# Performance work log

Measured on AMD Instinct MI355X. Metric: run time of the kernel, lower is better.

The kernel has to match this reference:

```python
import jax, jax.numpy as jnp
import numpy as np

N = 100000
IN_C, HID_C, OUT_C = 128, 128, 64
E = 1600000


def setup_inputs() -> dict:
    key = jax.random.key(0)
    ks = jax.random.split(key, 8)
    x = jax.random.normal(ks[0], (N, IN_C), dtype=jnp.float32)
    edge_index = jax.random.randint(ks[1], (2, E), 0, N, dtype=jnp.int64)
    def glorot(k, fan_in, fan_out):
        lim = np.sqrt(6.0 / (fan_in + fan_out)).astype(np.float32)
        return jax.random.uniform(k, (fan_in, fan_out), jnp.float32, -lim, lim)
    return {
        "x": x,
        "edge_index": edge_index,
        "W1l": glorot(ks[2], IN_C, HID_C),   # lin_l: aggregated neighbors
        "W1r": glorot(ks[3], IN_C, HID_C),   # lin_r: root/self
        "b1": jnp.zeros((HID_C,), jnp.float32),
        "W2l": glorot(ks[4], HID_C, OUT_C),
        "W2r": glorot(ks[5], HID_C, OUT_C),
        "b2": jnp.zeros((OUT_C,), jnp.float32),
    }


def _sage_conv(x, src, dst, Wl, Wr, b):
    # mean aggregation over incoming edges: gather source feats, segment-sum at dst
    msg_sum = jax.ops.segment_sum(x[src], dst, num_segments=N)          # [N, C_in]
    deg = jax.ops.segment_sum(jnp.ones((src.shape[0],), x.dtype), dst,
                              num_segments=N)                           # [N]
    mean = msg_sum / jnp.clip(deg, 1.0, None)[:, None]
    return mean @ Wl + x @ Wr + b


def reference(x, edge_index, W1l, W1r, b1, W2l, W2r, b2):
    src, dst = edge_index[0], edge_index[1]
    h = jax.nn.relu(_sage_conv(x, src, dst, W1l, W1r, b1))
    out = _sage_conv(h, src, dst, W2l, W2r, b2)
    return out
```

## Files before the change

### kernel.cpp

```cpp
#include <hip/hip_runtime.h>
#include <type_traits>


constexpr int K = 128;
constexpr int EB = 4096;

typedef __bf16 bf16x2 __attribute__((ext_vector_type(2)));
typedef __bf16 bf16x4 __attribute__((ext_vector_type(4)));
typedef __bf16 bf16x8 __attribute__((ext_vector_type(8)));
typedef float f32x4 __attribute__((ext_vector_type(4)));
typedef float f32x2 __attribute__((ext_vector_type(2)));


__device__ __forceinline__ unsigned char to_fp8(float v) {
#if __has_builtin(__builtin_amdgcn_cvt_pk_fp8_f32)
  int p = __builtin_amdgcn_cvt_pk_fp8_f32(v, v, 0, false);
  return (unsigned char)(p & 0xff);
#else
  unsigned u = __builtin_bit_cast(unsigned, v);
  unsigned s = (u >> 24) & 0x80u;
  float a = fabsf(v);
  if (a > 448.f) a = 448.f;
  unsigned bits;
  if (a < 0.015625f) {
    bits = (unsigned)(a * 512.f + 0.5f);
  } else {
    unsigned b = __builtin_bit_cast(unsigned, a);
    b += ((b >> 20) & 1) + 0x0007FFFF;
    unsigned e = (b >> 23) - 120;
    bits = (e << 3) | ((b >> 20) & 7);
    if (bits > 0x7E) bits = 0x7E;
  }
  return (unsigned char)(s | bits);
#endif
}

__device__ __forceinline__ f32x2 from_fp8x2(unsigned short u) {
#if __has_builtin(__builtin_amdgcn_cvt_pk_f32_fp8)
  return __builtin_amdgcn_cvt_pk_f32_fp8((int)u, false);
#else
  f32x2 r;
  unsigned b0 = u & 0xff, b1 = (u >> 8) & 0xff;
  unsigned e0 = (b0 >> 3) & 15, m0 = b0 & 7;
  unsigned e1 = (b1 >> 3) & 15, m1 = b1 & 7;
  float v0 = e0 ? __builtin_bit_cast(float, ((e0 + 120) << 23) | (m0 << 20))
              : (float)m0 * 0.001953125f;
  float v1 = e1 ? __builtin_bit_cast(float, ((e1 + 120) << 23) | (m1 << 20))
              : (float)m1 * 0.001953125f;
  r[0] = (b0 & 0x80) ? -v0 : v0;
  r[1] = (b1 & 0x80) ? -v1 : v1;
  return r;
#endif
}

__device__ __forceinline__ f32x2 fp8x2_lo(unsigned v) {
#if __has_builtin(__builtin_amdgcn_cvt_pk_f32_fp8)
  return __builtin_amdgcn_cvt_pk_f32_fp8((int)v, false);
#else
  return from_fp8x2((unsigned short)(v & 0xffffu));
#endif
}

__device__ __forceinline__ f32x2 fp8x2_hi(unsigned v) {
#if __has_builtin(__builtin_amdgcn_cvt_pk_f32_fp8)
  return __builtin_amdgcn_cvt_pk_f32_fp8((int)v, true);
#else
  return from_fp8x2((unsigned short)(v >> 16));
#endif
}


__global__ __launch_bounds__(256) void k_wprep_all(
    const float* __restrict__ W1l, const float* __restrict__ W1r,
    const float* __restrict__ W2l, const float* __restrict__ W2r,
    __bf16* __restrict__ B1l, __bf16* __restrict__ B1r,
    __bf16* __restrict__ B2l, __bf16* __restrict__ B2r) {
  int b = blockIdx.x;
  const float* W;
  __bf16* Bt;
  int idx;
  bool wide;
  if (b < 64) {
    W = W1l; Bt = B1l; idx = b * 256 + threadIdx.x; wide = true;
  } else if (b < 128) {
    W = W1r; Bt = B1r; idx = (b - 64) * 256 + threadIdx.x; wide = true;
  } else if (b < 160) {
    W = W2l; Bt = B2l; idx = (b - 128) * 256 + threadIdx.x; wide = false;
  } else {
    W = W2r; Bt = B2r; idx = (b - 160) * 256 + threadIdx.x; wide = false;
  }
  int k = wide ? (idx >> 7) : (idx >> 6);
  int c = wide ? (idx & 127) : (idx & 63);
  Bt[c * K + k] = (__bf16)W[idx];
}


__global__ __launch_bounds__(256) void k_bhist(const int* __restrict__ dst,
                                               int* __restrict__ blockHist,
                                               int* __restrict__ bucketTotal,
                                               int E, int n, int nB) {
  extern __shared__ int hist[];
  for (int i = threadIdx.x; i < nB; i += 256) hist[i] = 0;
  __syncthreads();
  int base = blockIdx.x * EB, end = min(base + EB, E);
  for (int e = base + threadIdx.x; e < end; e += 256) {
    int d = dst[e];
    if ((unsigned)d < (unsigned)n) atomicAdd(&hist[d >> 8], 1);
  }
  __syncthreads();
  for (int i = threadIdx.x; i < nB; i += 256) {
    int v = hist[i];
    blockHist[(long)blockIdx.x * nB + i] = v;
    if (v) atomicAdd(&bucketTotal[i], v);
  }
}

__global__ __launch_bounds__(512) void k_btop(const int* __restrict__ bucketTotal,
                                              int* __restrict__ bucketBase,
                                              int* __restrict__ bucketCursor, int nB) {
  __shared__ int sh[512];
  int t = threadIdx.x;
  int s = (t < nB) ? bucketTotal[t] : 0;
  sh[t] = s;
  __syncthreads();
  for (int off = 1; off < 512; off <<= 1) {
    int v = (t >= off) ? sh[t - off] : 0;
    __syncthreads();
    sh[t] += v;
    __syncthreads();
  }
  if (t < nB) {
    int base = sh[t] - s;
    bucketBase[t] = base;
    bucketCursor[t] = base;
    if (t == nB - 1) bucketBase[nB] = sh[t];
  }
}

__global__ __launch_bounds__(256) void k_bscatter(const int* __restrict__ src,
                                                  const int* __restrict__ dst,
                                                  const int* __restrict__ blockHist,
                                                  int* __restrict__ bucketCursor,
                                                  unsigned* __restrict__ recs,
                                                  int E, int n, int nB) {
  extern __shared__ int cur[];
  for (int i = threadIdx.x; i < nB; i += 256) {
    int c = blockHist[(long)blockIdx.x * nB + i];
    cur[i] = c ? atomicAdd(&bucketCursor[i], c) : 0;
  }
  __syncthreads();
  int base = blockIdx.x * EB, end = min(base + EB, E);
  for (int e = base + threadIdx.x; e < end; e += 256) {
    int d = dst[e];
    if ((unsigned)d < (unsigned)n) {
      int s = min(max(src[e], 0), n - 1);
      int pos = atomicAdd(&cur[d >> 8], 1);
      recs[pos] = ((unsigned)s << 8) | (unsigned)(d & 255);
    }
  }
}

__global__ __launch_bounds__(256) void k_bfill(const unsigned* __restrict__ recs,
                                               const int* __restrict__ bucketBase,
                                               int* __restrict__ rowptr,
                                               int* __restrict__ col, int n, int nB) {
  __shared__ int degl[256];
  __shared__ int incl[256];
  int b = blockIdx.x, t = threadIdx.x;
  int rbeg = bucketBase[b], rend = bucketBase[b + 1];
  degl[t] = 0;
  __syncthreads();
  for (int i = rbeg + t; i < rend; i += 256)
    atomicAdd(&degl[recs[i] & 255], 1);
  __syncthreads();
  incl[t] = degl[t];
  __syncthreads();
  for (int off = 1; off < 256; off <<= 1) {
    int v = (t >= off) ? incl[t - off] : 0;
    __syncthreads();
    incl[t] += v;
    __syncthreads();
  }
  int excl = incl[t] - degl[t];
  int node = b * 256 + t;
  if (node <= n) rowptr[node] = rbeg + excl;
  __syncthreads();
  degl[t] = rbeg + excl;
  __syncthreads();
  for (int i = rbeg + t; i < rend; i += 256) {
    unsigned r = recs[i];
    int pos = atomicAdd(&degl[r & 255], 1);
    col[pos] = (int)(r >> 8);
  }
}


template <int COLS, typename TIN>
__global__ __launch_bounds__(256) void k_gemm_fused(const TIN* __restrict__ X,
                                                    const __bf16* __restrict__ Bta,
                                                    const __bf16* __restrict__ Btb,
                                                    unsigned char* __restrict__ outA,
                                                    __bf16* __restrict__ outB, int nrows) {
  constexpr int LD = 136;
  constexpr int MT_N = COLS / 32;
  __shared__ __bf16 As[64 * LD];

  int tid = threadIdx.x;
  long row0 = (long)blockIdx.x * 64;

  if constexpr (std::is_same_v<TIN, float>) {
#pragma unroll
    for (int it = 0; it < 8; ++it) {
      int i = tid + it * 256;
      int r = i >> 5, c4 = (i & 31) << 2;
      long row = row0 + r;
      float4 v = make_float4(0.f, 0.f, 0.f, 0.f);
      if (row < nrows) v = *(const float4*)(X + row * K + c4);
      bf16x4 bb;
      bb[0] = (__bf16)v.x; bb[1] = (__bf16)v.y; bb[2] = (__bf16)v.z; bb[3] = (__bf16)v.w;
      *(bf16x4*)&As[r * LD + c4] = bb;
    }
  } else {
#pragma unroll
    for (int it = 0; it < 4; ++it) {
      int i = tid + it * 256;
      int r = i >> 4, c8 = (i & 15) << 3;
      long row = row0 + r;
      bf16x8 v = {};
      if (row < nrows) v = *(const bf16x8*)(X + row * K + c8);
      *(bf16x8*)&As[r * LD + c8] = v;
    }
  }
  __syncthreads();

  int w = tid >> 6, lane = tid & 63;
  int m = lane & 15, quad = lane >> 4;
  int wrow = (w >> 1) * 32;
  int wcol = (w & 1) * (COLS / 2);

#pragma unroll
  for (int p = 0; p < 2; ++p) {
    const __bf16* Btg = p ? Btb : Bta;

    f32x4 acc[2][MT_N];
#pragma unroll
    for (int mi = 0; mi < 2; ++mi)
#pragma unroll
      for (int ni = 0; ni < MT_N; ++ni) acc[mi][ni] = (f32x4){0.f, 0.f, 0.f, 0.f};

#pragma unroll
    for (int kc = 0; kc < 4; ++kc) {
      int ko = kc * 32 + quad * 8;
      bf16x8 af[2];
#pragma unroll
      for (int mi = 0; mi < 2; ++mi)
        af[mi] = *(const bf16x8*)&As[(wrow + mi * 16 + m) * LD + ko];
      bf16x8 bfr[MT_N];
#pragma unroll
      for (int ni = 0; ni < MT_N; ++ni)
        bfr[ni] = *(const bf16x8*)(Btg + (long)(wcol + ni * 16 + m) * K + ko);
#pragma unroll
      for (int mi = 0; mi < 2; ++mi)
#pragma unroll
        for (int ni = 0; ni < MT_N; ++ni)
          acc[mi][ni] = __builtin_amdgcn_mfma_f32_16x16x32_bf16(af[mi], bfr[ni], acc[mi][ni], 0, 0, 0);
    }

#pragma unroll
    for (int mi = 0; mi < 2; ++mi) {
#pragma unroll
      for (int r = 0; r < 4; ++r) {
        long grow = row0 + wrow + mi * 16 + quad * 4 + r;
        if (grow < nrows) {
#pragma unroll
          for (int ni = 0; ni < MT_N; ++ni) {
            long idx = grow * COLS + wcol + ni * 16 + m;
            float v = acc[mi][ni][r];
            if (p == 0) outA[idx] = to_fp8(v);
            else        outB[idx] = (__bf16)v;
          }
        }
      }
    }
  }
}


template <bool RELU>
__global__ __launch_bounds__(256) void k_agg128(const unsigned char* __restrict__ Y,
                                                const __bf16* __restrict__ XR,
                                                const float* __restrict__ bias,
                                                const int* __restrict__ rowptr,
                                                const int* __restrict__ col,
                                                __bf16* __restrict__ out, int nnodes) {
  int wave = threadIdx.x >> 6, lane = threadIdx.x & 63;
  int quarter = lane >> 4, l = lane & 15;
  int sb = lane & 48;
  int n = blockIdx.x * 16 + wave * 4 + quarter;
  bool valid = n < nnodes;
  int beg = 0, end = 0;
  if (valid) {
    beg = rowptr[n];
    end = rowptr[n + 1];
  }
  int co = l * 8;
  const unsigned char* Yc = Y + co;

  f32x2 av0 = {0.f, 0.f}, av1 = {0.f, 0.f}, av2 = {0.f, 0.f}, av3 = {0.f, 0.f};

  for (int base = beg; base < end; base += 16) {
    int cnt = min(end - base, 16);
    int idx = (l < cnt) ? col[base + l] : 0;
    int j = 0;
    for (; j + 3 < cnt; j += 4) {
      long s0 = (unsigned)__shfl(idx, sb + j);
      long s1 = (unsigned)__shfl(idx, sb + j + 1);
      long s2 = (unsigned)__shfl(idx, sb + j + 2);
      long s3 = (unsigned)__shfl(idx, sb + j + 3);
      uint2 v0 = *(const uint2*)(Yc + s0 * 128);
      uint2 v1 = *(const uint2*)(Yc + s1 * 128);
      uint2 v2 = *(const uint2*)(Yc + s2 * 128);
      uint2 v3 = *(const uint2*)(Yc + s3 * 128);
      av0 += fp8x2_lo(v0.x); av1 += fp8x2_hi(v0.x);
      av2 += fp8x2_lo(v0.y); av3 += fp8x2_hi(v0.y);
      av0 += fp8x2_lo(v1.x); av1 += fp8x2_hi(v1.x);
      av2 += fp8x2_lo(v1.y); av3 += fp8x2_hi(v1.y);
      av0 += fp8x2_lo(v2.x); av1 += fp8x2_hi(v2.x);
      av2 += fp8x2_lo(v2.y); av3 += fp8x2_hi(v2.y);
      av0 += fp8x2_lo(v3.x); av1 += fp8x2_hi(v3.x);
      av2 += fp8x2_lo(v3.y); av3 += fp8x2_hi(v3.y);
    }
    for (; j < cnt; ++j) {
      long s = (unsigned)__shfl(idx, sb + j);
      uint2 v = *(const uint2*)(Yc + s * 128);
      av0 += fp8x2_lo(v.x); av1 += fp8x2_hi(v.x);
      av2 += fp8x2_lo(v.y); av3 += fp8x2_hi(v.y);
    }
  }

  if (valid) {
    float inv = 1.f / (float)max(end - beg, 1);
    bf16x8 xv = *(const bf16x8*)(XR + (long)n * 128 + co);
    f32x4 b0 = *(const f32x4*)(bias + co);
    f32x4 b1 = *(const f32x4*)(bias + co + 4);
    float r0 = av0[0] * inv + (float)xv[0] + b0[0];
    float r1 = av0[1] * inv + (float)xv[1] + b0[1];
    float r2 = av1[0] * inv + (float)xv[2] + b0[2];
    float r3 = av1[1] * inv + (float)xv[3] + b0[3];
    float r4 = av2[0] * inv + (float)xv[4] + b1[0];
    float r5 = av2[1] * inv + (float)xv[5] + b1[1];
    float r6 = av3[0] * inv + (float)xv[6] + b1[2];
    float r7 = av3[1] * inv + (float)xv[7] + b1[3];
    if (RELU) {
      r0 = fmaxf(r0, 0.f); r1 = fmaxf(r1, 0.f);
      r2 = fmaxf(r2, 0.f); r3 = fmaxf(r3, 0.f);
      r4 = fmaxf(r4, 0.f); r5 = fmaxf(r5, 0.f);
      r6 = fmaxf(r6, 0.f); r7 = fmaxf(r7, 0.f);
    }
    bf16x8 o;
    o[0] = (__bf16)r0; o[1] = (__bf16)r1; o[2] = (__bf16)r2; o[3] = (__bf16)r3;
    o[4] = (__bf16)r4; o[5] = (__bf16)r5; o[6] = (__bf16)r6; o[7] = (__bf16)r7;
    *(bf16x8*)(out + (long)n * 128 + co) = o;
  }
}

__global__ __launch_bounds__(256) void k_agg64(const unsigned char* __restrict__ Y,
                                               const __bf16* __restrict__ XR,
                                               const float* __restrict__ bias,
                                               const int* __restrict__ rowptr,
                                               const int* __restrict__ col,
                                               float* __restrict__ out, int nnodes) {
  int wave = threadIdx.x >> 6, lane = threadIdx.x & 63;
  int quarter = lane >> 4, l = lane & 15;
  int sb = lane & 48;
  int n = blockIdx.x * 16 + wave * 4 + quarter;
  bool valid = n < nnodes;
  int beg = 0, end = 0;
  if (valid) {
    beg = rowptr[n];
    end = rowptr[n + 1];
  }
  int co = l * 4;
  const unsigned char* Yc = Y + co;

  f32x2 av0 = {0.f, 0.f}, av1 = {0.f, 0.f};

  for (int base = beg; base < end; base += 16) {
    int cnt = min(end - base, 16);
    int idx = (l < cnt) ? col[base + l] : 0;
    int j = 0;
    for (; j + 3 < cnt; j += 4) {
      long s0 = (unsigned)__shfl(idx, sb + j);
      long s1 = (unsigned)__shfl(idx, sb + j + 1);
      long s2 = (unsigned)__shfl(idx, sb + j + 2);
      long s3 = (unsigned)__shfl(idx, sb + j + 3);
      unsigned v0 = *(const unsigned*)(Yc + s0 * 64);
      unsigned v1 = *(const unsigned*)(Yc + s1 * 64);
      unsigned v2 = *(const unsigned*)(Yc + s2 * 64);
      unsigned v3 = *(const unsigned*)(Yc + s3 * 64);
      av0 += fp8x2_lo(v0); av1 += fp8x2_hi(v0);
      av0 += fp8x2_lo(v1); av1 += fp8x2_hi(v1);
      av0 += fp8x2_lo(v2); av1 += fp8x2_hi(v2);
      av0 += fp8x2_lo(v3); av1 += fp8x2_hi(v3);
    }
    for (; j < cnt; ++j) {
      long s = (unsigned)__shfl(idx, sb + j);
      unsigned v = *(const unsigned*)(Yc + s * 64);
      av0 += fp8x2_lo(v); av1 += fp8x2_hi(v);
    }
  }

  if (valid) {
    float inv = 1.f / (float)max(end - beg, 1);
    bf16x4 xv = *(const bf16x4*)(XR + (long)n * 64 + co);
    f32x4 bv = *(const f32x4*)(bias + co);
    f32x4 r;
    r[0] = av0[0] * inv + (float)xv[0] + bv[0];
    r[1] = av0[1] * inv + (float)xv[1] + bv[1];
    r[2] = av1[0] * inv + (float)xv[2] + bv[2];
    r[3] = av1[1] * inv + (float)xv[3] + bv[3];
    *(f32x4*)(out + (long)n * 64 + co) = r;
  }
}


extern "C" void kernel_launch(void* const* d_in, const int* in_sizes, int n_in,
                              void* d_out, int out_size, void* d_ws, size_t ws_size,
                              hipStream_t stream) {
  const float* x   = (const float*)d_in[0];
  const int*   ei  = (const int*)d_in[1];
  const float* W1l = (const float*)d_in[2];
  const float* W1r = (const float*)d_in[3];
  const float* b1  = (const float*)d_in[4];
  const float* W2l = (const float*)d_in[5];
  const float* W2r = (const float*)d_in[6];
  const float* b2  = (const float*)d_in[7];
  float* out = (float*)d_out;

  int N = in_sizes[0] / K;
  int E = in_sizes[1] / 2;
  const int* src = ei;
  const int* dst = ei + E;

  int nB = (N + 255) >> 8;
  int nblk = (E + EB - 1) / EB;

  char* ws = (char*)d_ws;
  size_t off = 0;
  auto alloc = [&](size_t bytes) {
    void* p = ws + off;
    off = (off + bytes + 255) & ~(size_t)255;
    return p;
  };
  int*      rowptr       = (int*)alloc(((size_t)N + 2) * 4);
  int*      col          = (int*)alloc((size_t)E * 4);
  int*      blockHist    = (int*)alloc((size_t)nblk * nB * 4);
  int*      bucketTotal  = (int*)alloc(((size_t)nB) * 4);
  int*      bucketBase   = (int*)alloc(((size_t)nB + 1) * 4);
  int*      bucketCursor = (int*)alloc((size_t)nB * 4);
  unsigned* recs         = (unsigned*)alloc((size_t)E * 4);
  unsigned char* y1      = (unsigned char*)alloc((size_t)N * 128);
  __bf16*   xr           = (__bf16*)alloc((size_t)N * 128 * 2);
  __bf16*   h            = (__bf16*)alloc((size_t)N * 128 * 2);
  __bf16*   Bt1l         = (__bf16*)alloc((size_t)128 * K * 2);
  __bf16*   Bt1r         = (__bf16*)alloc((size_t)128 * K * 2);
  __bf16*   Bt2l         = (__bf16*)alloc((size_t)64 * K * 2);
  __bf16*   Bt2r         = (__bf16*)alloc((size_t)64 * K * 2);
  unsigned char* y2 = y1;
  __bf16*   hr = xr;

  k_wprep_all<<<192, 256, 0, stream>>>(W1l, W1r, W2l, W2r, Bt1l, Bt1r, Bt2l, Bt2r);

  hipMemsetAsync(bucketTotal, 0, (size_t)nB * 4, stream);
  k_bhist<<<nblk, 256, nB * 4, stream>>>(dst, blockHist, bucketTotal, E, N, nB);
  k_btop<<<1, 512, 0, stream>>>(bucketTotal, bucketBase, bucketCursor, nB);
  k_bscatter<<<nblk, 256, nB * 4, stream>>>(src, dst, blockHist, bucketCursor, recs, E, N, nB);
  k_bfill<<<nB, 256, 0, stream>>>(recs, bucketBase, rowptr, col, N, nB);

  int gx = (N + 63) / 64;
  k_gemm_fused<128, float><<<gx, 256, 0, stream>>>(x, Bt1l, Bt1r, y1, xr, N);
  k_agg128<true><<<(N + 15) / 16, 256, 0, stream>>>(y1, xr, b1, rowptr, col, h, N);

  k_gemm_fused<64, __bf16><<<gx, 256, 0, stream>>>(h, Bt2l, Bt2r, y2, hr, N);
  k_agg64<<<(N + 15) / 16, 256, 0, stream>>>(y2, hr, b2, rowptr, col, out, N);
}
```

Before: 288.0 us.

## Split GEMM waves across weight panels and preload B fragments into registers

The fused dual-GEMM kernel now gives each block 32 rows instead of 64. Instead of every wave looping over both weight matrices, half the waves compute the lin_l panel (fp8 output) and half compute the lin_r panel (bf16 output). Each wave loads all its B fragments into registers up front, before the A tile is staged, and launch bounds are raised to request 4 blocks per CU. This aims to raise occupancy, overlap the weight loads with the A staging, and remove the serial two-pass loop, at the cost of more registers per thread and twice as many blocks that each reload the weights.

```diff
diff --git a/kernel.cpp b/kernel.cpp
--- a/kernel.cpp
+++ b/kernel.cpp
@@ -196,21 +196,34 @@
 
 
 template <int COLS, typename TIN>
-__global__ __launch_bounds__(256) void k_gemm_fused(const TIN* __restrict__ X,
-                                                    const __bf16* __restrict__ Bta,
-                                                    const __bf16* __restrict__ Btb,
-                                                    unsigned char* __restrict__ outA,
-                                                    __bf16* __restrict__ outB, int nrows) {
+__global__ __launch_bounds__(256, 4) void k_gemm_fused(const TIN* __restrict__ X,
+                                                       const __bf16* __restrict__ Bta,
+                                                       const __bf16* __restrict__ Btb,
+                                                       unsigned char* __restrict__ outA,
+                                                       __bf16* __restrict__ outB, int nrows) {
   constexpr int LD = 136;
-  constexpr int MT_N = COLS / 32;
-  __shared__ __bf16 As[64 * LD];
+  constexpr int NI = COLS / 32;
+  __shared__ __bf16 As[32 * LD];
 
   int tid = threadIdx.x;
-  long row0 = (long)blockIdx.x * 64;
+  long row0 = (long)blockIdx.x * 32;
+
+  int w = tid >> 6, lane = tid & 63;
+  int m = lane & 15, quad = lane >> 4;
+  int panel = w >> 1;
+  int wcol = (w & 1) * (COLS / 2);
+  const __bf16* Btg = panel ? Btb : Bta;
+
+  bf16x8 bq[4][NI];
+#pragma unroll
+  for (int kc = 0; kc < 4; ++kc)
+#pragma unroll
+    for (int ni = 0; ni < NI; ++ni)
+      bq[kc][ni] = *(const bf16x8*)(Btg + (long)(wcol + ni * 16 + m) * K + kc * 32 + quad * 8);
 
   if constexpr (std::is_same_v<TIN, float>) {
 #pragma unroll
-    for (int it = 0; it < 8; ++it) {
+    for (int it = 0; it < 4; ++it) {
       int i = tid + it * 256;
       int r = i >> 5, c4 = (i & 31) << 2;
       long row = row0 + r;
@@ -222,7 +235,7 @@
     }
   } else {
 #pragma unroll
-    for (int it = 0; it < 4; ++it) {
+    for (int it = 0; it < 2; ++it) {
       int i = tid + it * 256;
       int r = i >> 4, c8 = (i & 15) << 3;
       long row = row0 + r;
@@ -233,52 +246,38 @@
   }
   __syncthreads();
 
-  int w = tid >> 6, lane = tid & 63;
-  int m = lane & 15, quad = lane >> 4;
-  int wrow = (w >> 1) * 32;
-  int wcol = (w & 1) * (COLS / 2);
-
-#pragma unroll
-  for (int p = 0; p < 2; ++p) {
-    const __bf16* Btg = p ? Btb : Bta;
-
-    f32x4 acc[2][MT_N];
+  f32x4 acc[2][NI];
+#pragma unroll
+  for (int mi = 0; mi < 2; ++mi)
+#pragma unroll
+    for (int ni = 0; ni < NI; ++ni) acc[mi][ni] = (f32x4){0.f, 0.f, 0.f, 0.f};
+
+#pragma unroll
+  for (int kc = 0; kc < 4; ++kc) {
+    int ko = kc * 32 + quad * 8;
+    bf16x8 af[2];
 #pragma unroll
     for (int mi = 0; mi < 2; ++mi)
-#pragma unroll
-      for (int ni = 0; ni < MT_N; ++ni) acc[mi][ni] = (f32x4){0.f, 0.f, 0.f, 0.f};
-
-#pragma unroll
-    for (int kc = 0; kc < 4; ++kc) {
-      int ko = kc * 32 + quad * 8;
-      bf16x8 af[2];
-#pragma unroll
-      for (int mi = 0; mi < 2; ++mi)
-        af[mi] = *(const bf16x8*)&As[(wrow + mi * 16 + m) * LD + ko];
-      bf16x8 bfr[MT_N];
-#pragma unroll
-      for (int ni = 0; ni < MT_N; ++ni)
-        bfr[ni] = *(const bf16x8*)(Btg + (long)(wcol + ni * 16 + m) * K + ko);
-#pragma unroll
-      for (int mi = 0; mi < 2; ++mi)
-#pragma unroll
-        for (int ni = 0; ni < MT_N; ++ni)
-          acc[mi][ni] = __builtin_amdgcn_mfma_f32_16x16x32_bf16(af[mi], bfr[ni], acc[mi][ni], 0, 0, 0);
-    }
-
-#pragma unroll
-    for (int mi = 0; mi < 2; ++mi) {
-#pragma unroll
-      for (int r = 0; r < 4; ++r) {
-        long grow = row0 + wrow + mi * 16 + quad * 4 + r;
-        if (grow < nrows) {
-#pragma unroll
-          for (int ni = 0; ni < MT_N; ++ni) {
-            long idx = grow * COLS + wcol + ni * 16 + m;
-            float v = acc[mi][ni][r];
-            if (p == 0) outA[idx] = to_fp8(v);
-            else        outB[idx] = (__bf16)v;
-          }
+      af[mi] = *(const bf16x8*)&As[(mi * 16 + m) * LD + ko];
+#pragma unroll
+    for (int mi = 0; mi < 2; ++mi)
+#pragma unroll
+      for (int ni = 0; ni < NI; ++ni)
+        acc[mi][ni] = __builtin_amdgcn_mfma_f32_16x16x32_bf16(af[mi], bq[kc][ni], acc[mi][ni], 0, 0, 0);
+  }
+
+#pragma unroll
+  for (int mi = 0; mi < 2; ++mi) {
+#pragma unroll
+    for (int r = 0; r < 4; ++r) {
+      long grow = row0 + mi * 16 + quad * 4 + r;
+      if (grow < nrows) {
+#pragma unroll
+        for (int ni = 0; ni < NI; ++ni) {
+          long idx = grow * COLS + wcol + ni * 16 + m;
+          float v = acc[mi][ni][r];
+          if (panel == 0) outA[idx] = to_fp8(v);
+          else            outB[idx] = (__bf16)v;
         }
       }
     }
@@ -477,7 +476,7 @@
   k_bscatter<<<nblk, 256, nB * 4, stream>>>(src, dst, blockHist, bucketCursor, recs, E, N, nB);
   k_bfill<<<nB, 256, 0, stream>>>(recs, bucketBase, rowptr, col, N, nB);
 
-  int gx = (N + 63) / 64;
+  int gx = (N + 31) / 32;
   k_gemm_fused<128, float><<<gx, 256, 0, stream>>>(x, Bt1l, Bt1r, y1, xr, N);
   k_agg128<true><<<(N + 15) / 16, 256, 0, stream>>>(y1, xr, b1, rowptr, col, h, N);
 
```

Measured after the change: 285.2 us. Within noise of the previous version (-1.0%).
